# Kernel tuning notes

Hardware: AMD Instinct MI355X
Metric: run time of the kernel (lower is better)

## Reference

```python
import jax, jax.numpy as jnp
import numpy as np

BS, GS, D, KMAX = 256, 1024, 128, 4
VRANGE = 6.0
NEG = -1e30


def _u(key, shape, fan):
    s = 1.0 / np.sqrt(fan)
    return jax.random.uniform(key, shape, jnp.float32, -s, s)


def _gru(x, hp, Wih, Whh, bih, bhh):
    # torch.nn.GRUCell math
    gi = x @ Wih.T + bih
    gh = hp @ Whh.T + bhh
    ir, iz, inn = jnp.split(gi, 3, axis=-1)
    hr, hz, hn = jnp.split(gh, 3, axis=-1)
    r = jax.nn.sigmoid(ir + hr)
    z = jax.nn.sigmoid(iz + hz)
    n = jnp.tanh(inn + r * hn)
    return (1.0 - z) * n + z * hp


def _gather_h(h, idx):  # h [B,G,D], idx [B,1] -> [B,D]
    B, G, Dd = h.shape
    return jnp.take_along_axis(h, jnp.broadcast_to(idx[:, :, None], (B, 1, Dd)), axis=1)[:, 0]


def setup_inputs() -> dict:
    key = jax.random.key(0)
    ks = jax.random.split(key, 32)
    p = {}
    for i, n in enumerate(["K1", "K2", "K3", "K4", "Q1", "Q2", "Q3", "Q4"]):
        p["W_" + n] = _u(ks[i], (D, D), D)
    p["meta_W1"] = _u(ks[8], (8, 9), 9)
    p["meta_b1"] = _u(ks[9], (8,), 9)
    p["meta_W2"] = _u(ks[10], (2 * D, 8), 8)
    p["meta_b2"] = _u(ks[11], (2 * D,), 8)
    p["init_hidden_W"] = _u(ks[12], (D, D), D)
    p["init_hidden_b"] = _u(ks[13], (D,), D)
    p["init_query"] = _u(ks[14], (D,), D)
    for j, r in enumerate(["rnn1", "rnn2"]):
        p[r + "_Wih"] = _u(ks[15 + 4 * j], (3 * D, D), D)
        p[r + "_Whh"] = _u(ks[16 + 4 * j], (3 * D, D), D)
        p[r + "_bih"] = _u(ks[17 + 4 * j], (3 * D,), D)
        p[r + "_bhh"] = _u(ks[18 + 4 * j], (3 * D,), D)
    inp = dict(
        h=jax.random.normal(ks[24], (BS, GS, D), jnp.float32),
        context2=jax.random.normal(ks[25], (BS, 9), jnp.float32),
        rec=jax.random.randint(ks[26], (BS, GS), 0, GS),
        visited_time=jax.random.randint(ks[27], (BS, GS), 0, GS),
        last_action=jax.random.randint(ks[28], (BS, 1), 0, GS),
        fixed_action=jax.random.randint(ks[29], (BS, KMAX), 0, GS),
        k_max=KMAX,
    )
    inp.update(p)
    return inp


def reference(h, context2, rec, visited_time, last_action, fixed_action, k_max,
              W_K1, W_K2, W_K3, W_K4, W_Q1, W_Q2, W_Q3, W_Q4,
              meta_W1, meta_b1, meta_W2, meta_b2,
              init_hidden_W, init_hidden_b, init_query,
              rnn1_Wih, rnn1_Whh, rnn1_bih, rnn1_bhh,
              rnn2_Wih, rnn2_Whh, rnn2_bih, rnn2_bhh):
    bs, gs, d = h.shape
    # with_feature3: meta_linear(context2) -> [V1, V2]
    hid = jax.nn.relu(context2 @ meta_W1.T + meta_b1)
    lv = hid @ meta_W2.T + meta_b2
    V1, V2 = lv[:, :d], lv[:, d:]
    h_mean = h.mean(1)
    q1 = h_mean @ init_hidden_W.T + init_hidden_b
    q2 = q1
    input_q1 = jnp.broadcast_to(init_query[None, :], (bs, d))
    input_q2 = input_q1
    # K-projections are step-invariant; precompute (same math as in-loop linear_K)
    K1h = h @ W_K1.T
    K2h = h @ W_K2.T
    K3h = h @ W_K3.T
    K4h = h @ W_K4.T
    mask = jnp.zeros((bs, gs), bool)
    stopped = jnp.ones((bs,), bool)
    nola = jnp.full((bs, 1), -1, rec.dtype)  # next_of_last_action
    action_index = jnp.zeros((bs, k_max), rec.dtype)
    kal = jnp.zeros((bs, k_max + 1), rec.dtype)
    kar = jnp.zeros((bs, k_max), rec.dtype)
    ll = jnp.zeros((bs,), h.dtype)
    cols = jnp.arange(gs)[None, :]
    vtt = None
    for i in range(k_max):
        q1 = _gru(input_q1, q1, rnn1_Wih, rnn1_Whh, rnn1_bih, rnn1_bhh)
        q2 = _gru(input_q2, q2, rnn2_Wih, rnn2_Whh, rnn2_bih, rnn2_bhh)
        t1 = jnp.tanh(K1h + (q1 @ W_Q1.T)[:, None, :] + K3h * (q1 @ W_Q3.T)[:, None, :])
        t2 = jnp.tanh(K2h + (q2 @ W_Q2.T)[:, None, :] + K4h * (q2 @ W_Q4.T)[:, None, :])
        result = jnp.einsum('bgd,bd->bg', t1, V1) + jnp.einsum('bgd,bd->bg', t2, V2)
        logits = jnp.tanh(result) * VRANGE
        logits = jnp.where(mask, NEG, logits)
        if i == 0:
            logits = jnp.where(cols == last_action[:, :1], NEG, logits)
        action = fixed_action[:, i:i + 1]
        if i > 0:
            action = jnp.where(stopped[:, None], action_index[:, :1], action)
        logp = jax.nn.log_softmax(logits, axis=-1)
        loss_now = jnp.take_along_axis(logp, action, axis=1)[:, 0]
        ll = ll + (jnp.where(stopped, 0.0, loss_now) if i > 0 else loss_now)
        nona = jnp.take_along_axis(rec, action, axis=1)  # next_of_new_action
        a = action[:, 0]
        action_index = action_index.at[:, i].set(a)
        kal = kal.at[:, i].set(jnp.where(stopped, a, kal[:, i]))
        jprev = (i - 1) % k_max
        kar = kar.at[:, jprev].set(jnp.where(~stopped, a, kar[:, jprev]))
        kal = kal.at[:, i + 1].set(nona[:, 0])
        input_q1 = _gather_h(h, action)
        input_q2 = jnp.where(stopped[:, None], input_q1, _gather_h(h, nola % gs))
        hit = (action == nola)[:, 0]
        stopped = (stopped | hit) if i > 0 else hit
        kal = kal.at[:, i].set(jnp.where(stopped, kal[:, (i - 1) % (k_max + 1)], kal[:, i]))
        kar = kar.at[:, i].set(jnp.where(stopped, kar[:, jprev], kar[:, i]))
        if i == 0:
            vtt = (visited_time - jnp.take_along_axis(visited_time, action, axis=1)) % gs
        vtt_a = jnp.take_along_axis(vtt, action, axis=1)
        mask = vtt <= vtt_a
        if i == 0:
            mask = mask | (vtt > gs - 2)
        mask = jnp.where(stopped[:, None] & (cols == action), False, mask)
        allow = (~stopped) & (nona[:, 0] == action_index[:, 0])
        mask = jnp.where(allow[:, None] & (cols == action_index[:, :1]), False, mask)
        nola = jnp.where(stopped[:, None], jnp.array(-1, rec.dtype), nona)
    kar = kar.at[:, -1].set(jnp.where(~stopped, kal[:, -1], kar[:, -1]))
    action_all = jnp.concatenate([action_index, kal[:, :k_max], kar], axis=-1)
    return action_all, ll
```

## Files before the change

kernel.cpp:

```cpp
#include <hip/hip_runtime.h>
#include <hip/hip_bf16.h>
#include <math.h>

#define GS 1024
#define BSZ 256
#define DD 128
#define NEGV -1e30f

typedef __attribute__((ext_vector_type(8))) short bf16x8_t;
typedef __attribute__((ext_vector_type(4))) float f32x4_t;
typedef __attribute__((ext_vector_type(2))) float f32x2_t;

#define WGRU_OFF_BYTES 131072
#define WQP_OFF_BYTES  524288
#define WIHB_OFF_BYTES 655360
#define F_OFF_BYTES    688128
#define FH_HM   0
#define FI_V    262144
#define FJ_AQB  327680
#define FK_RES  851968
#define F_TOTAL 1900544
#define DESC_OFF_BYTES (F_OFF_BYTES + F_TOTAL * 4)
#define HBF_OFF_BYTES  (DESC_OFF_BYTES + 32768)
#define WS_NEED ((size_t)HBF_OFF_BYTES + (size_t)BSZ * GS * DD * 2)

__device__ __forceinline__ float rtanh(float x) {
    float s = fmaf(x, x, 1.0f);
    return x * __builtin_amdgcn_rsqf(s);
}
__device__ __forceinline__ float tanh2(float x) {
    float e = __expf(x + x);
    return fmaf(-2.0f, __builtin_amdgcn_rcpf(e + 1.0f), 1.0f);
}
__device__ __forceinline__ float sigm2(float x) {
    return __builtin_amdgcn_rcpf(1.0f + __expf(-x));
}
__device__ __forceinline__ unsigned short f2bf(float f) {
    union { float f; unsigned u; } v; v.f = f;
    unsigned u = v.u;
    return (unsigned short)((u + 0x7fffu + ((u >> 16) & 1u)) >> 16);
}
#define MFMA16(a, b, c) __builtin_amdgcn_mfma_f32_16x16x32_bf16((a), (b), (c), 0, 0, 0)

__global__ __launch_bounds__(128) void init_kernel(
    const float* __restrict__ h,
    const float* __restrict__ wk1, const float* __restrict__ wk2,
    const float* __restrict__ wk3, const float* __restrict__ wk4,
    const float* __restrict__ wq1, const float* __restrict__ wq2,
    const float* __restrict__ wq3, const float* __restrict__ wq4,
    const float* __restrict__ ihw,
    const float* __restrict__ r1ih, const float* __restrict__ r1hh,
    const float* __restrict__ r2ih, const float* __restrict__ r2hh,
    unsigned short* __restrict__ wbf, unsigned short* __restrict__ wgru,
    unsigned short* __restrict__ wqp, unsigned short* __restrict__ wihb,
    float* __restrict__ F, unsigned short* __restrict__ hbf, int use_hbf)
{
    if (blockIdx.x < 2048) {
        int b = blockIdx.x >> 3, seg = blockIdx.x & 7, d = threadIdx.x;
        size_t rowbase = (size_t)(b * GS + seg * 128);
        const float* base = h + rowbase * DD + d;
        float s = 0.0f;
        if (use_hbf) {
            unsigned short* ob = hbf + rowbase * DD + d;
#pragma unroll 8
            for (int r = 0; r < 128; r++) {
                float v = base[(size_t)r * DD];
                s += v;
                ob[(size_t)r * DD] = f2bf(v);
            }
        } else {
#pragma unroll 8
            for (int r = 0; r < 128; r++) s += base[(size_t)r * DD];
        }
        F[FH_HM + b * 1024 + seg * 128 + d] = s;
        return;
    }
    int tid = (blockIdx.x - 2048) * 128 + threadIdx.x;
    int nth = 128 * 128;
    const float* wks[4]  = {wk1, wk2, wk3, wk4};
    const float* rws[4]  = {r1ih, r1hh, r2ih, r2hh};
    const float* wqs2[4] = {wq1, wq3, wq2, wq4};

    for (int e = tid; e < 65536; e += nth)
        wbf[e] = f2bf(wks[e >> 14][e & 16383]);
    for (int e = tid; e < 196608; e += nth)
        wgru[e] = f2bf(rws[e / 49152][e % 49152]);
    for (int e = tid; e < 65536; e += nth)
        wqp[e] = f2bf(wqs2[e >> 14][e & 16383]);
    for (int e = tid; e < 16384; e += nth)
        wihb[e] = f2bf(ihw[e]);
}

__global__ __launch_bounds__(512) void prep_kernel(
    const float* __restrict__ h, const float* __restrict__ ctx2,
    const int* __restrict__ rec, const int* __restrict__ vt,
    const int* __restrict__ la_, const int* __restrict__ fa,
    const float* __restrict__ mW1, const float* __restrict__ mb1,
    const float* __restrict__ mW2, const float* __restrict__ mb2,
    const float* __restrict__ ihb, const float* __restrict__ iq,
    const float* __restrict__ b1ih, const float* __restrict__ b1hh,
    const float* __restrict__ b2ih, const float* __restrict__ b2hh,
    const unsigned short* __restrict__ wgru, const unsigned short* __restrict__ wqp,
    const unsigned short* __restrict__ wihb,
    float* __restrict__ F, int* __restrict__ DESC, float* __restrict__ out)
{
    int rho = blockIdx.x & 1;
    int b0  = (blockIdx.x >> 1) * 16;
    int t = threadIdx.x;
    int lane = t & 63, w = t >> 6, ml = lane & 15, quad = lane >> 4;
    int dloc = w * 16 + ml;

    __shared__ __attribute__((aligned(16))) unsigned short hmb[16][136];
    __shared__ __attribute__((aligned(16))) unsigned short Xall[4][16][136];
    __shared__ __attribute__((aligned(16))) unsigned short Qb[2][16][136];
    __shared__ float hid[16][8];
    __shared__ int sdesc[16][26];

    const float* bih = rho ? b2ih : b1ih;
    const float* bhh = rho ? b2hh : b1hh;

#pragma unroll
    for (int k = 0; k < 4; k++) {
        int e = t + 512 * k;
        int b = e >> 7, d = e & 127;
        float s = 0.0f;
#pragma unroll
        for (int seg = 0; seg < 8; seg++)
            s += F[FH_HM + (b0 + b) * 1024 + seg * 128 + d];
        hmb[b][d] = f2bf(s * (1.0f / 1024.0f));
    }
    if (t < 128) {
        int b = t >> 3, u = t & 7;
        float a = mb1[u];
        for (int k = 0; k < 9; k++) a += mW1[u * 9 + k] * ctx2[(b0 + b) * 9 + k];
        hid[b][u] = a > 0.0f ? a : 0.0f;
    }
    if (t >= 128 && t < 144) {
        int tb = t - 128;
        int b = b0 + tb;
        int ai[4], kal[5] = {0, 0, 0, 0, 0}, kar[4] = {0, 0, 0, 0};
        int idesc[26];
        int stopped = 1, nola = -1, vt0 = 0;
        for (int i = 0; i < 4; i++) {
            idesc[16 + i] = stopped;
            idesc[22 + i] = nola;
            int action = fa[b * 4 + i];
            if (i > 0 && stopped) action = ai[0];
            int nona = rec[b * GS + action];
            ai[i] = action;
            if (stopped) kal[i] = action;
            int jprev = (i + 3) & 3;
            if (!stopped) kar[jprev] = action;
            kal[i + 1] = nona;
            int hit = (action == nola) ? 1 : 0;
            int st = (i > 0) ? (stopped | hit) : hit;
            if (st) kal[i] = kal[(i + 4) % 5];
            if (st) kar[i] = kar[jprev];
            if (i == 0) vt0 = vt[b * GS + action];
            idesc[0 + i]  = action;
            idesc[4 + i]  = (vt[b * GS + action] - vt0) & (GS - 1);
            idesc[8 + i]  = st;
            idesc[12 + i] = (!st && (nona == ai[0])) ? 1 : 0;
            nola = st ? -1 : nona;
            stopped = st;
        }
        if (!stopped) kar[3] = kal[4];
        idesc[20] = la_[b];
        idesc[21] = vt0;
        int* dd = DESC + b * 32;
        for (int c = 0; c < 26; c++) { dd[c] = idesc[c]; sdesc[tb][c] = idesc[c]; }
        float* oa = out + b * 12;
        for (int c = 0; c < 4; c++) {
            oa[c]     = (float)ai[c];
            oa[4 + c] = (float)kal[c];
            oa[8 + c] = (float)kar[c];
        }
    }
    __syncthreads();

#pragma unroll
    for (int k = 0; k < 8; k++) {
        int o = t + 512 * k;
        int b = o >> 8, idx = o & 255;
        float a = mb2[idx];
#pragma unroll
        for (int u = 0; u < 8; u++) a += mW2[idx * 8 + u] * hid[b][u];
        F[FI_V + (b0 + b) * 256 + idx] = a;
    }
    for (int e = t; e < 2048; e += 512) {
        int row = e >> 7, d = e & 127;
        Xall[0][row][d] = f2bf(iq[d]);
    }
    for (int e = t; e < 6144; e += 512) {
        int i = (e >> 11) + 1;
        int b = (e >> 7) & 15, d = e & 127;
        int a = sdesc[b][i - 1];
        int srcrow = a;
        if (rho) {
            int sE = sdesc[b][16 + (i - 1)];
            int nl = sdesc[b][22 + (i - 1)];
            srcrow = sE ? a : (nl & (GS - 1));
        }
        Xall[i][b][d] = f2bf(h[((size_t)((b0 + b) * GS + srcrow)) * DD + d]);
    }
    float qreg[4];
    {
        bf16x8_t am[4];
#pragma unroll
        for (int kt = 0; kt < 4; kt++)
            am[kt] = *(const bf16x8_t*)&hmb[ml][kt * 32 + quad * 8];
        const unsigned short* wb = wihb + (size_t)dloc * 128 + quad * 8;
        f32x4_t acc = {0.f, 0.f, 0.f, 0.f};
#pragma unroll
        for (int kt = 0; kt < 4; kt++)
            acc = MFMA16(am[kt], *(const bf16x8_t*)(wb + kt * 32), acc);
        float bias = ihb[dloc];
#pragma unroll
        for (int r_ = 0; r_ < 4; r_++) {
            qreg[r_] = acc[r_] + bias;
            Qb[0][quad * 4 + r_][dloc] = f2bf(qreg[r_]);
        }
    }
    __syncthreads();

    float bir = bih[dloc], biz = bih[128 + dloc], bin_ = bih[256 + dloc];
    float bhr = bhh[dloc], bhz = bhh[128 + dloc], bhn = bhh[256 + dloc];

    for (int i = 0; i < 4; i++) {
        int cur = i & 1;
        bf16x8_t ax[4], aq[4];
#pragma unroll
        for (int kt = 0; kt < 4; kt++) {
            ax[kt] = *(const bf16x8_t*)&Xall[i][ml][kt * 32 + quad * 8];
            aq[kt] = *(const bf16x8_t*)&Qb[cur][ml][kt * 32 + quad * 8];
        }
        f32x4_t gi[3], gh[3];
#pragma unroll
        for (int gate = 0; gate < 3; gate++) {
            int n = gate * 128 + dloc;
            const unsigned short* wi = wgru + ((size_t)((rho * 2 + 0) * 384 + n)) * 128 + quad * 8;
            const unsigned short* wh = wgru + ((size_t)((rho * 2 + 1) * 384 + n)) * 128 + quad * 8;
            f32x4_t ai = {0.f, 0.f, 0.f, 0.f}, ah = {0.f, 0.f, 0.f, 0.f};
#pragma unroll
            for (int kt = 0; kt < 4; kt++) {
                ai = MFMA16(ax[kt], *(const bf16x8_t*)(wi + kt * 32), ai);
                ah = MFMA16(aq[kt], *(const bf16x8_t*)(wh + kt * 32), ah);
            }
            gi[gate] = ai; gh[gate] = ah;
        }
#pragma unroll
        for (int r_ = 0; r_ < 4; r_++) {
            float r = sigm2(gi[0][r_] + bir + gh[0][r_] + bhr);
            float z = sigm2(gi[1][r_] + biz + gh[1][r_] + bhz);
            float n = tanh2(gi[2][r_] + bin_ + r * (gh[2][r_] + bhn));
            qreg[r_] = fmaf(z, qreg[r_] - n, n);
            Qb[cur ^ 1][quad * 4 + r_][dloc] = f2bf(qreg[r_]);
        }
        __syncthreads();

        bf16x8_t aqn[4];
#pragma unroll
        for (int kt = 0; kt < 4; kt++)
            aqn[kt] = *(const bf16x8_t*)&Qb[cur ^ 1][ml][kt * 32 + quad * 8];
#pragma unroll
        for (int half = 0; half < 2; half++) {
            int nrow = half * 128 + dloc;
            const unsigned short* wq = wqp + ((size_t)(rho * 256 + nrow)) * 128 + quad * 8;
            f32x4_t acc = {0.f, 0.f, 0.f, 0.f};
#pragma unroll
            for (int kt = 0; kt < 4; kt++)
                acc = MFMA16(aqn[kt], *(const bf16x8_t*)(wq + kt * 32), acc);
            int sel = rho * 2 + half;
#pragma unroll
            for (int r_ = 0; r_ < 4; r_++) {
                int b2 = b0 + quad * 4 + r_;
                F[FJ_AQB + b2 * 2048 + dloc * 16 + i * 4 + sel] = acc[r_];
            }
        }
    }
}

#define LOADA(dst, TL) do {                                                    \
    if (HBF) {                                                                 \
        _Pragma("unroll")                                                      \
        for (int kt = 0; kt < 4; kt++)                                         \
            dst[kt] = *(const bf16x8_t*)(ab + (size_t)(TL) * 2048 + kt * 32);  \
    } else {                                                                   \
        _Pragma("unroll")                                                      \
        for (int kt = 0; kt < 4; kt++) {                                       \
            f32x4_t lo = *(const f32x4_t*)(fb + (size_t)(TL) * 2048 + kt * 32);     \
            f32x4_t hi = *(const f32x4_t*)(fb + (size_t)(TL) * 2048 + kt * 32 + 4); \
            union { unsigned short s[8]; bf16x8_t v; } pk_;                    \
            pk_.s[0] = f2bf(lo[0]); pk_.s[1] = f2bf(lo[1]);                    \
            pk_.s[2] = f2bf(lo[2]); pk_.s[3] = f2bf(lo[3]);                    \
            pk_.s[4] = f2bf(hi[0]); pk_.s[5] = f2bf(hi[1]);                    \
            pk_.s[6] = f2bf(hi[2]); pk_.s[7] = f2bf(hi[3]);                    \
            dst[kt] = pk_.v;                                                   \
        }                                                                      \
    }                                                                          \
} while (0)

#define COMPUTE(TL, af) do {                                                   \
    f32x4_t c[4];                                                              \
    _Pragma("unroll") for (int m_ = 0; m_ < 4; m_++)                           \
        c[m_] = (f32x4_t){0.f, 0.f, 0.f, 0.f};                                 \
    _Pragma("unroll") for (int kt = 0; kt < 4; kt++) {                         \
        _Pragma("unroll") for (int m_ = 0; m_ < 4; m_++)                       \
            c[m_] = MFMA16(af[kt], bfr[m_][kt], c[m_]);                        \
    }                                                                          \
    float v[16];                                                               \
    _Pragma("unroll") for (int r_ = 0; r_ < 4; r_++) {                         \
        f32x2_t cA = {c[0][r_], c[1][r_]};                                     \
        f32x2_t cM = {c[2][r_], c[3][r_]};                                     \
        _Pragma("unroll") for (int j_ = 0; j_ < 4; j_++) {                     \
            f32x2_t y = cA + aa[j_] + cM * bb[j_];                             \
            f32x2_t s = y * y + (f32x2_t){1.0f, 1.0f};                         \
            f32x2_t rs = {__builtin_amdgcn_rsqf(s[0]), __builtin_amdgcn_rsqf(s[1])}; \
            f32x2_t tv = y * rs * VV;                                          \
            v[r_ * 4 + j_] = tv[0] + tv[1];                                    \
        }                                                                      \
    }                                                                          \
    { int bs = ml & 1;                                                         \
      _Pragma("unroll") for (int i_ = 0; i_ < 8; i_++) {                       \
          float lo = v[2 * i_], hi = v[2 * i_ + 1];                            \
          float send = bs ? lo : hi; float recv = __shfl_xor(send, 1);         \
          v[i_] = (bs ? hi : lo) + recv; } }                                   \
    { int bs = (ml >> 1) & 1;                                                  \
      _Pragma("unroll") for (int i_ = 0; i_ < 4; i_++) {                       \
          float lo = v[2 * i_], hi = v[2 * i_ + 1];                            \
          float send = bs ? lo : hi; float recv = __shfl_xor(send, 2);         \
          v[i_] = (bs ? hi : lo) + recv; } }                                   \
    { int bs = (ml >> 2) & 1;                                                  \
      _Pragma("unroll") for (int i_ = 0; i_ < 2; i_++) {                       \
          float lo = v[2 * i_], hi = v[2 * i_ + 1];                            \
          float send = bs ? lo : hi; float recv = __shfl_xor(send, 4);         \
          v[i_] = (bs ? hi : lo) + recv; } }                                   \
    { int bs = (ml >> 3) & 1;                                                  \
      float lo = v[0], hi = v[1];                                              \
      float send = bs ? lo : hi; float recv = __shfl_xor(send, 8);             \
      v[0] = (bs ? hi : lo) + recv; }                                          \
    atomicAdd(&red[TL][quad * 16 + ml], v[0]);                                 \
} while (0)

template<int HBF>
__global__ __launch_bounds__(512, 2) void score_kernel(
    const float* __restrict__ h, const unsigned short* __restrict__ hbf,
    const unsigned short* __restrict__ wbf, float* __restrict__ F)
{
    int b = blockIdx.x >> 2, gq = blockIdx.x & 3;
    int t = threadIdx.x;
    int lane = t & 63, w = t >> 6;
    int ml = lane & 15, quad = lane >> 4;
    int dg = w * 16 + ml;

    __shared__ float red[16][64];
    for (int e = t; e < 1024; e += 512) ((float*)red)[e] = 0.0f;

    bf16x8_t bfr[4][4];
#pragma unroll
    for (int mat = 0; mat < 4; mat++)
#pragma unroll
        for (int kt = 0; kt < 4; kt++)
            bfr[mat][kt] = *(const bf16x8_t*)(wbf + ((size_t)(mat * 128 + dg)) * 128 + kt * 32 + quad * 8);
#pragma unroll
    for (int mat = 0; mat < 4; mat++)
#pragma unroll
        for (int kt = 0; kt < 4; kt++)
            asm volatile("" : "+v"(bfr[mat][kt]));

    const float* Vb = F + FI_V + b * 256;
    f32x2_t VV = {Vb[dg], Vb[128 + dg]};
    const float* AQ = F + FJ_AQB + b * 2048 + dg * 16;
    f32x2_t aa[4], bb[4];
#pragma unroll
    for (int j = 0; j < 4; j++) {
        f32x4_t q = *(const f32x4_t*)(AQ + j * 4);
        aa[j] = (f32x2_t){q[0], q[2]};
        bb[j] = (f32x2_t){q[1], q[3]};
    }

    __syncthreads();

    int grow0 = gq * 256;
    const unsigned short* ab = hbf + ((size_t)(b * GS + grow0) + ml) * 128 + quad * 8;
    const float*          fb = h   + ((size_t)(b * GS + grow0) + ml) * 128 + quad * 8;

    bf16x8_t afA[4], afB[4];
    LOADA(afA, 0);
#pragma unroll
    for (int tp = 0; tp < 8; tp++) {
        LOADA(afB, 2 * tp + 1);
        COMPUTE(2 * tp, afA);
        if (tp < 7) LOADA(afA, 2 * tp + 2);
        COMPUTE(2 * tp + 1, afB);
    }
    __syncthreads();

    for (int e = t; e < 1024; e += 512) {
        int j = e >> 8, gl = e & 255;
        int tl = gl >> 4, row = gl & 15;
        float val = red[tl][(row >> 2) * 16 + (row & 3) * 4 + j];
        F[FK_RES + (size_t)b * 4096 + j * 1024 + grow0 + gl] = val;
    }
}

__global__ __launch_bounds__(256) void finalize_kernel(
    const float* __restrict__ F, const int* __restrict__ DESC,
    const int* __restrict__ vt, float* __restrict__ out)
{
    int b = blockIdx.x, t = threadIdx.x;
    const int* dd = DESC + b * 32;
    int act0 = dd[0], la = dd[20], vt0 = dd[21];
    __shared__ float sred[8];
    __shared__ float schosen;
    float ll = 0.0f;

    int vtts[4];
#pragma unroll
    for (int q = 0; q < 4; q++) {
        int g = t + q * 256;
        vtts[q] = (vt[b * GS + g] - vt0) & (GS - 1);
    }

    for (int j = 0; j < 4; j++) {
        int aj = dd[j];
        float lg[4];
#pragma unroll
        for (int q = 0; q < 4; q++) {
            int g = t + q * 256;
            bool neg;
            if (j == 0) {
                neg = (g == la);
            } else {
                int p = j - 1;
                neg = (vtts[q] <= dd[4 + p]) || (p == 0 && vtts[q] > GS - 2);
                if (dd[8 + p] && g == dd[p]) neg = false;
                if (dd[12 + p] && g == act0) neg = false;
            }
            float r = F[FK_RES + (size_t)b * 4096 + j * 1024 + g];
            float vv = neg ? NEGV : 6.0f * rtanh(r);
            lg[q] = vv;
            if (g == aj) schosen = vv;
        }
        float mx = fmaxf(fmaxf(lg[0], lg[1]), fmaxf(lg[2], lg[3]));
#pragma unroll
        for (int o = 1; o < 64; o <<= 1) mx = fmaxf(mx, __shfl_xor(mx, o));
        if ((t & 63) == 0) sred[t >> 6] = mx;
        __syncthreads();
        mx = fmaxf(fmaxf(sred[0], sred[1]), fmaxf(sred[2], sred[3]));
        float sm = 0.0f;
#pragma unroll
        for (int q = 0; q < 4; q++) sm += __expf(lg[q] - mx);
#pragma unroll
        for (int o = 1; o < 64; o <<= 1) sm += __shfl_xor(sm, o);
        if ((t & 63) == 0) sred[4 + (t >> 6)] = sm;
        __syncthreads();
        if (t == 0) {
            float tot = sred[4] + sred[5] + sred[6] + sred[7];
            float lse = mx + logf(tot);
            int gate = (j == 0) || (!dd[16 + j]);
            if (gate) ll += schosen - lse;
        }
        __syncthreads();
    }
    if (t == 0) out[3072 + b] = ll;
}

extern "C" void kernel_launch(void* const* d_in, const int* in_sizes, int n_in,
                              void* d_out, int out_size, void* d_ws, size_t ws_size,
                              hipStream_t stream)
{
    (void)in_sizes; (void)n_in; (void)out_size;
    const float* h    = (const float*)d_in[0];
    const float* ctx2 = (const float*)d_in[1];
    const int*   rec  = (const int*)d_in[2];
    const int*   vtm  = (const int*)d_in[3];
    const int*   la   = (const int*)d_in[4];
    const int*   fa   = (const int*)d_in[5];
    const float* wk1 = (const float*)d_in[7];
    const float* wk2 = (const float*)d_in[8];
    const float* wk3 = (const float*)d_in[9];
    const float* wk4 = (const float*)d_in[10];
    const float* wq1 = (const float*)d_in[11];
    const float* wq2 = (const float*)d_in[12];
    const float* wq3 = (const float*)d_in[13];
    const float* wq4 = (const float*)d_in[14];
    const float* mW1 = (const float*)d_in[15];
    const float* mb1 = (const float*)d_in[16];
    const float* mW2 = (const float*)d_in[17];
    const float* mb2 = (const float*)d_in[18];
    const float* ihw = (const float*)d_in[19];
    const float* ihb = (const float*)d_in[20];
    const float* iq  = (const float*)d_in[21];
    const float* r1ih = (const float*)d_in[22];
    const float* r1hh = (const float*)d_in[23];
    const float* b1ih = (const float*)d_in[24];
    const float* b1hh = (const float*)d_in[25];
    const float* r2ih = (const float*)d_in[26];
    const float* r2hh = (const float*)d_in[27];
    const float* b2ih = (const float*)d_in[28];
    const float* b2hh = (const float*)d_in[29];

    unsigned short* wbf  = (unsigned short*)d_ws;
    unsigned short* wgru = (unsigned short*)((char*)d_ws + WGRU_OFF_BYTES);
    unsigned short* wqp  = (unsigned short*)((char*)d_ws + WQP_OFF_BYTES);
    unsigned short* wihb = (unsigned short*)((char*)d_ws + WIHB_OFF_BYTES);
    float* F   = (float*)((char*)d_ws + F_OFF_BYTES);
    int* DESC  = (int*)((char*)d_ws + DESC_OFF_BYTES);
    unsigned short* hbf = (unsigned short*)((char*)d_ws + HBF_OFF_BYTES);
    float* out = (float*)d_out;

    int use_hbf = (ws_size >= WS_NEED) ? 1 : 0;

    init_kernel<<<dim3(2176), dim3(128), 0, stream>>>(h, wk1, wk2, wk3, wk4,
                                                      wq1, wq2, wq3, wq4, ihw,
                                                      r1ih, r1hh, r2ih, r2hh,
                                                      wbf, wgru, wqp, wihb, F,
                                                      hbf, use_hbf);
    prep_kernel<<<dim3(32), dim3(512), 0, stream>>>(h, ctx2, rec, vtm, la, fa,
                                                    mW1, mb1, mW2, mb2, ihb, iq,
                                                    b1ih, b1hh, b2ih, b2hh,
                                                    wgru, wqp, wihb, F, DESC, out);
    if (use_hbf)
        score_kernel<1><<<dim3(1024), dim3(512), 0, stream>>>(h, hbf, wbf, F);
    else
        score_kernel<0><<<dim3(1024), dim3(512), 0, stream>>>(h, hbf, wbf, F);
    finalize_kernel<<<dim3(256), dim3(256), 0, stream>>>(F, DESC, vtm, out);
}
```

Baseline: 424.2 us.

## Store bf16 h in MFMA fragment order with vectorized conversion and sum

The init kernel now reads h with 16-byte vector loads, converts to bf16 and writes it in a tile/kt/lane-swizzled layout matching the MFMA A-fragment order. Column sums go through a shared-memory reduction. The score kernel then loads fragments contiguously per lane, giving fully coalesced 16-byte accesses, and launch_bounds asks for 4 blocks per CU instead of 2. The higher occupancy target may force register spills given the 64 preloaded bf16 weight fragments per thread.

Result: slower. 527.4 us (+24.3%).

```diff
diff --git a/kernel.cpp b/kernel.cpp
--- a/kernel.cpp
+++ b/kernel.cpp
@@ -53,25 +53,43 @@
     const float* __restrict__ r2ih, const float* __restrict__ r2hh,
     unsigned short* __restrict__ wbf, unsigned short* __restrict__ wgru,
     unsigned short* __restrict__ wqp, unsigned short* __restrict__ wihb,
-    float* __restrict__ F, unsigned short* __restrict__ hbf, int use_hbf)
+    float* __restrict__ F, unsigned short* __restrict__ hbw, int use_hbf)
 {
     if (blockIdx.x < 2048) {
-        int b = blockIdx.x >> 3, seg = blockIdx.x & 7, d = threadIdx.x;
-        size_t rowbase = (size_t)(b * GS + seg * 128);
-        const float* base = h + rowbase * DD + d;
+        int b = blockIdx.x >> 3, seg = blockIdx.x & 7;
+        int t = threadIdx.x;
+        int rg = t >> 4, c = t & 15;
+        int kt = c >> 2, quad = c & 3;
+        float s0=0.f,s1=0.f,s2=0.f,s3=0.f,s4=0.f,s5=0.f,s6=0.f,s7=0.f;
+#pragma unroll
+        for (int i = 0; i < 16; i++) {
+            int rl = rg + 8 * i;
+            const float* src = h + ((size_t)(b * GS + seg * 128 + rl)) * DD + c * 8;
+            f32x4_t lo = *(const f32x4_t*)src;
+            f32x4_t hi = *(const f32x4_t*)(src + 4);
+            s0 += lo[0]; s1 += lo[1]; s2 += lo[2]; s3 += lo[3];
+            s4 += hi[0]; s5 += hi[1]; s6 += hi[2]; s7 += hi[3];
+            if (use_hbf) {
+                int T = seg * 8 + (rl >> 4), ml = rl & 15;
+                union { unsigned short s[8]; bf16x8_t v; } pk;
+                pk.s[0] = f2bf(lo[0]); pk.s[1] = f2bf(lo[1]);
+                pk.s[2] = f2bf(lo[2]); pk.s[3] = f2bf(lo[3]);
+                pk.s[4] = f2bf(hi[0]); pk.s[5] = f2bf(hi[1]);
+                pk.s[6] = f2bf(hi[2]); pk.s[7] = f2bf(hi[3]);
+                size_t off = ((((size_t)(b * 64 + T)) * 4 + kt) * 64 + quad * 16 + ml) * 8;
+                *(bf16x8_t*)(hbw + off) = pk.v;
+            }
+        }
+        __shared__ float cs[8][128];
+        cs[rg][c * 8 + 0] = s0; cs[rg][c * 8 + 1] = s1;
+        cs[rg][c * 8 + 2] = s2; cs[rg][c * 8 + 3] = s3;
+        cs[rg][c * 8 + 4] = s4; cs[rg][c * 8 + 5] = s5;
+        cs[rg][c * 8 + 6] = s6; cs[rg][c * 8 + 7] = s7;
+        __syncthreads();
+        int d = t;
         float s = 0.0f;
-        if (use_hbf) {
-            unsigned short* ob = hbf + rowbase * DD + d;
-#pragma unroll 8
-            for (int r = 0; r < 128; r++) {
-                float v = base[(size_t)r * DD];
-                s += v;
-                ob[(size_t)r * DD] = f2bf(v);
-            }
-        } else {
-#pragma unroll 8
-            for (int r = 0; r < 128; r++) s += base[(size_t)r * DD];
-        }
+#pragma unroll
+        for (int k = 0; k < 8; k++) s += cs[k][d];
         F[FH_HM + b * 1024 + seg * 128 + d] = s;
         return;
     }
@@ -284,7 +302,7 @@
     if (HBF) {                                                                 \
         _Pragma("unroll")                                                      \
         for (int kt = 0; kt < 4; kt++)                                         \
-            dst[kt] = *(const bf16x8_t*)(ab + (size_t)(TL) * 2048 + kt * 32);  \
+            dst[kt] = *(const bf16x8_t*)(ab + (size_t)(TL) * 2048 + kt * 512); \
     } else {                                                                   \
         _Pragma("unroll")                                                      \
         for (int kt = 0; kt < 4; kt++) {                                       \
@@ -343,8 +361,8 @@
 } while (0)
 
 template<int HBF>
-__global__ __launch_bounds__(512, 2) void score_kernel(
-    const float* __restrict__ h, const unsigned short* __restrict__ hbf,
+__global__ __launch_bounds__(512, 4) void score_kernel(
+    const float* __restrict__ h, const unsigned short* __restrict__ hbw,
     const unsigned short* __restrict__ wbf, float* __restrict__ F)
 {
     int b = blockIdx.x >> 2, gq = blockIdx.x & 3;
@@ -382,7 +400,7 @@
     __syncthreads();
 
     int grow0 = gq * 256;
-    const unsigned short* ab = hbf + ((size_t)(b * GS + grow0) + ml) * 128 + quad * 8;
+    const unsigned short* ab = hbw + ((size_t)(b * 64 + gq * 16)) * 2048 + (size_t)lane * 8;
     const float*          fb = h   + ((size_t)(b * GS + grow0) + ml) * 128 + quad * 8;
 
     bf16x8_t afA[4], afB[4];
@@ -507,7 +525,7 @@
     unsigned short* wihb = (unsigned short*)((char*)d_ws + WIHB_OFF_BYTES);
     float* F   = (float*)((char*)d_ws + F_OFF_BYTES);
     int* DESC  = (int*)((char*)d_ws + DESC_OFF_BYTES);
-    unsigned short* hbf = (unsigned short*)((char*)d_ws + HBF_OFF_BYTES);
+    unsigned short* hbw = (unsigned short*)((char*)d_ws + HBF_OFF_BYTES);
     float* out = (float*)d_out;
 
     int use_hbf = (ws_size >= WS_NEED) ? 1 : 0;
@@ -516,14 +534,14 @@
                                                       wq1, wq2, wq3, wq4, ihw,
                                                       r1ih, r1hh, r2ih, r2hh,
                                                       wbf, wgru, wqp, wihb, F,
-                                                      hbf, use_hbf);
+                                                      hbw, use_hbf);
     prep_kernel<<<dim3(32), dim3(512), 0, stream>>>(h, ctx2, rec, vtm, la, fa,
                                                     mW1, mb1, mW2, mb2, ihb, iq,
                                                     b1ih, b1hh, b2ih, b2hh,
                                                     wgru, wqp, wihb, F, DESC, out);
     if (use_hbf)
-        score_kernel<1><<<dim3(1024), dim3(512), 0, stream>>>(h, hbf, wbf, F);
+        score_kernel<1><<<dim3(1024), dim3(512), 0, stream>>>(h, hbw, wbf, F);
     else
-        score_kernel<0><<<dim3(1024), dim3(512), 0, stream>>>(h, hbf, wbf, F);
+        score_kernel<0><<<dim3(1024), dim3(512), 0, stream>>>(h, hbw, wbf, F);
     finalize_kernel<<<dim3(256), dim3(256), 0, stream>>>(F, DESC, vtm, out);
 }
```
